# Kernel optimization log

Hardware: AMD Instinct MI355X
Metric: run time of the kernel (lower is better)

## Reference

```python
import jax, jax.numpy as jnp
import numpy as np

NG = 1024      # graphs
NPG = 128      # nodes per graph (forced by lin1 = Linear(128*hid, 128))
N = NG * NPG   # 131072 nodes
DEG = 16       # avg in-graph degree
E = N * DEG    # 2,097,152 edges
IN, H = 4, 64


def setup_inputs() -> dict:
    key = jax.random.key(0)
    ks = jax.random.split(key, 24)
    x = jax.random.normal(ks[0], (N, IN), jnp.float32)
    # edges constrained within each 128-node graph
    src = jax.random.randint(ks[1], (E,), 0, NPG)
    dst = jax.random.randint(ks[2], (E,), 0, NPG)
    off = jnp.repeat(jnp.arange(NG, dtype=jnp.int32) * NPG, NPG * DEG)
    edge_index = jnp.stack([src.astype(jnp.int32) + off, dst.astype(jnp.int32) + off])
    g = lambda k, shp, fan: jax.random.normal(k, shp, jnp.float32) / np.float32(np.sqrt(fan))
    return {
        "x": x, "edge_index": edge_index,
        # GATv2Conv(4->64)
        "Wl": g(ks[3], (IN, H), IN), "bl": jnp.zeros((H,), jnp.float32),
        "Wr": g(ks[4], (IN, H), IN), "br": jnp.zeros((H,), jnp.float32),
        "att_v2": g(ks[5], (H,), H), "b_v2": jnp.zeros((H,), jnp.float32),
        # GATConv #1 (64->64)
        "Wg1": g(ks[6], (H, H), H), "as1": g(ks[7], (H,), H),
        "ad1": g(ks[8], (H,), H), "bg1": jnp.zeros((H,), jnp.float32),
        # GATConv #2 (64->64)
        "Wg2": g(ks[9], (H, H), H), "as2": g(ks[10], (H,), H),
        "ad2": g(ks[11], (H,), H), "bg2": jnp.zeros((H,), jnp.float32),
        # LayerNorm(64)
        "ln_g": jnp.ones((H,), jnp.float32), "ln_b": jnp.zeros((H,), jnp.float32),
        # heads: Linear(128*64 -> 128), Linear(128 -> 1)
        "W1": g(ks[12], (NPG * H, 128), NPG * H), "b1": jnp.zeros((128,), jnp.float32),
        "W2": g(ks[13], (128, 1), 128), "b2": jnp.zeros((1,), jnp.float32),
    }


def _seg_softmax(logits, seg):
    # stable softmax over edges grouped by destination node
    m = jax.ops.segment_max(logits, seg, num_segments=N)
    ex = jnp.exp(logits - m[seg])
    s = jax.ops.segment_sum(ex, seg, num_segments=N)
    return ex / (s[seg] + 1e-16)


def _gatv2(x, src, dst, Wl, bl, Wr, br, att, bias):
    xl = x @ Wl + bl                       # source transform [N,H]
    xr = x @ Wr + br                       # target transform [N,H]
    e = jax.nn.leaky_relu(xl[src] + xr[dst], 0.2) @ att   # [E]
    a = _seg_softmax(e, dst)
    out = jax.ops.segment_sum(a[:, None] * xl[src], dst, num_segments=N)
    return out + bias


def _gat(x, src, dst, W, a_src, a_dst, bias):
    # GATConv default: add self-loops
    loop = jnp.arange(N, dtype=src.dtype)
    s2 = jnp.concatenate([src, loop]); d2 = jnp.concatenate([dst, loop])
    xw = x @ W                             # [N,H]
    al_s = xw @ a_src; al_d = xw @ a_dst   # per-node attention halves [N]
    e = jax.nn.leaky_relu(al_s[s2] + al_d[d2], 0.2)
    a = _seg_softmax(e, d2)
    out = jax.ops.segment_sum(a[:, None] * xw[s2], d2, num_segments=N)
    return out + bias


def _layernorm(x, g, b, eps=1e-5):
    mu = jnp.mean(x, -1, keepdims=True)
    var = jnp.mean(jnp.square(x - mu), -1, keepdims=True)
    return (x - mu) * jax.lax.rsqrt(var + eps) * g + b


def reference(x, edge_index, Wl, bl, Wr, br, att_v2, b_v2,
              Wg1, as1, ad1, bg1, Wg2, as2, ad2, bg2,
              ln_g, ln_b, W1, b1, W2, b2):
    src, dst = edge_index[0], edge_index[1]
    h = jax.nn.leaky_relu(_gatv2(x, src, dst, Wl, bl, Wr, br, att_v2, b_v2), 0.01)
    h = _layernorm(h, ln_g, ln_b)
    h = jax.nn.relu(_gat(h, src, dst, Wg1, as1, ad1, bg1))
    h = jax.nn.relu(_gat(h, src, dst, Wg2, as2, ad2, bg2))
    # linearize: batch is sorted with exactly NPG nodes per graph -> reshape
    h = h.reshape(NG, NPG * H)
    h = jax.nn.leaky_relu(h @ W1 + b1, 0.01)
    return jax.nn.sigmoid(h @ W2 + b2)     # [NG, 1]
```

## Files before the change

kernel.cpp:

```cpp
#include <hip/hip_runtime.h>
#include <hip/hip_bf16.h>

#define NGRAPH 1024
#define NPG 128
#define NTOT (NGRAPH*NPG)
#define EPG 2048
#define ETOT (NTOT*16)
#define HD 64

typedef unsigned int uint;
typedef unsigned short ushort_t;
typedef __attribute__((ext_vector_type(8))) short s8v;
typedef __attribute__((ext_vector_type(4))) float f32x4;

#define MFMA16 __builtin_amdgcn_mfma_f32_16x16x32_bf16

__device__ __forceinline__ float lrelu(float x, float s){ return fmaxf(x, x*s); }
__device__ __forceinline__ float b2lo(uint u){ return __uint_as_float(u << 16); }
__device__ __forceinline__ float b2hi(uint u){ return __uint_as_float(u & 0xFFFF0000u); }
__device__ __forceinline__ uint pkbf(float a, float b){
  union { __hip_bfloat162 h; uint u; } t;
  t.h = __hip_bfloat162{__float2bfloat16(a), __float2bfloat16(b)};
  return t.u;
}
__device__ __forceinline__ ushort_t bfb(float v){
  __hip_bfloat16 h = __float2bfloat16(v);
  union { __hip_bfloat16 h; ushort_t u; } t; t.h = h; return t.u;
}
union U4S8 { uint4 u; s8v s; };
__device__ __forceinline__ s8v bcs8(uint4 u){ U4S8 t; t.u = u; return t.s; }

#define DPP_ADD(v, ctrl) ((v) + __int_as_float(__builtin_amdgcn_update_dpp(0, __float_as_int(v), (ctrl), 0xF, 0xF, false)))

__device__ __forceinline__ int oswz(int r, int p){ return (r<<5) | ((((p>>2) ^ (r & 7))<<2) | (p & 3)); }
__device__ __forceinline__ int obase(int r, int oc){ return (r<<5) | (((oc) ^ (r & 7))<<2); }

#define O_F   0
#define O_W   4096
#define O_EV  6144
#define O_ED  7168
#define O_X   8192
#define O_SOF 8704
#define O_SPO 8833
#define O_NMV 8961
#define O_SSE 9089
#define O_ALS 9217
#define O_ALD 9345
#define O_WAS 9476
#define O_WAD 9540
#define SM_SZ 9604

#define GF32A(s, a) { \
    uint4 q0 = *(uint4*)&SM[O_F + obase((s), 4*hf+0)]; \
    uint4 q1 = *(uint4*)&SM[O_F + obase((s), 4*hf+1)]; \
    c0.x += (a)*b2lo(q0.x); c0.y += (a)*b2hi(q0.x); c0.z += (a)*b2lo(q0.y); c0.w += (a)*b2hi(q0.y); \
    c1.x += (a)*b2lo(q0.z); c1.y += (a)*b2hi(q0.z); c1.z += (a)*b2lo(q0.w); c1.w += (a)*b2hi(q0.w); \
    c2.x += (a)*b2lo(q1.x); c2.y += (a)*b2hi(q1.x); c2.z += (a)*b2lo(q1.y); c2.w += (a)*b2hi(q1.y); \
    c3.x += (a)*b2lo(q1.z); c3.y += (a)*b2hi(q1.z); c3.z += (a)*b2lo(q1.w); c3.w += (a)*b2hi(q1.w); }
#define GF32B(s, a) { \
    uint4 q2 = *(uint4*)&SM[O_F + obase((s), 4*hf+2)]; \
    uint4 q3 = *(uint4*)&SM[O_F + obase((s), 4*hf+3)]; \
    c4.x += (a)*b2lo(q2.x); c4.y += (a)*b2hi(q2.x); c4.z += (a)*b2lo(q2.y); c4.w += (a)*b2hi(q2.y); \
    c5.x += (a)*b2lo(q2.z); c5.y += (a)*b2hi(q2.z); c5.z += (a)*b2lo(q2.w); c5.w += (a)*b2hi(q2.w); \
    c6.x += (a)*b2lo(q3.x); c6.y += (a)*b2hi(q3.x); c6.z += (a)*b2lo(q3.y); c6.w += (a)*b2hi(q3.y); \
    c7.x += (a)*b2lo(q3.z); c7.y += (a)*b2hi(q3.z); c7.z += (a)*b2lo(q3.w); c7.w += (a)*b2hi(q3.w); }
#define GF32(s, a) { GF32A(s, a) __builtin_amdgcn_sched_barrier(0); GF32B(s, a) }

#define STF32(d) { \
    sXl[oswz((d), hf*16+ 0)] = pkbf(c0.x, c0.y); sXl[oswz((d), hf*16+ 1)] = pkbf(c0.z, c0.w); \
    sXl[oswz((d), hf*16+ 2)] = pkbf(c1.x, c1.y); sXl[oswz((d), hf*16+ 3)] = pkbf(c1.z, c1.w); \
    sXl[oswz((d), hf*16+ 4)] = pkbf(c2.x, c2.y); sXl[oswz((d), hf*16+ 5)] = pkbf(c2.z, c2.w); \
    sXl[oswz((d), hf*16+ 6)] = pkbf(c3.x, c3.y); sXl[oswz((d), hf*16+ 7)] = pkbf(c3.z, c3.w); \
    sXl[oswz((d), hf*16+ 8)] = pkbf(c4.x, c4.y); sXl[oswz((d), hf*16+ 9)] = pkbf(c4.z, c4.w); \
    sXl[oswz((d), hf*16+10)] = pkbf(c5.x, c5.y); sXl[oswz((d), hf*16+11)] = pkbf(c5.z, c5.w); \
    sXl[oswz((d), hf*16+12)] = pkbf(c6.x, c6.y); sXl[oswz((d), hf*16+13)] = pkbf(c6.z, c6.w); \
    sXl[oswz((d), hf*16+14)] = pkbf(c7.x, c7.y); sXl[oswz((d), hf*16+15)] = pkbf(c7.z, c7.w); }

__global__ void __launch_bounds__(256) gnn_fused(
    const float* __restrict__ x, const int* __restrict__ ei,
    const float* __restrict__ Wl, const float* __restrict__ bl,
    const float* __restrict__ Wr, const float* __restrict__ br,
    const float* __restrict__ att, const float* __restrict__ bv2,
    const float* __restrict__ Wg1, const float* __restrict__ as1,
    const float* __restrict__ ad1, const float* __restrict__ bg1,
    const float* __restrict__ Wg2, const float* __restrict__ as2,
    const float* __restrict__ ad2, const float* __restrict__ bg2,
    const float* __restrict__ lng, const float* __restrict__ lnb,
    uint* __restrict__ hout)
{
  __shared__ uint SM[SM_SZ];
  uint*      sXl  = SM + O_F;
  _Float16*  evh  = (_Float16*)(SM + O_EV);
  ushort_t*  edsd = (ushort_t*)(SM + O_ED);
  int*       soff = (int*)(SM + O_SOF);
  int*       spos = (int*)(SM + O_SPO);
  float*     nmv  = (float*)(SM + O_NMV);
  float*     sse  = (float*)(SM + O_SSE);
  float*     als  = (float*)(SM + O_ALS);
  float*     ald  = (float*)(SM + O_ALD);
  float*     was  = (float*)(SM + O_WAS);
  float*     wad  = (float*)(SM + O_WAD);
  ushort_t*  sH16 = (ushort_t*)(SM + O_F);
  ushort_t*  wg16 = (ushort_t*)(SM + O_W);
  float*     lgf  = (float*)(SM + O_W);

  const int g    = blockIdx.x;
  const int tid  = threadIdx.x;
  const int lane = tid & 63;
  const int wv   = tid >> 6;
  const int lw   = lane & 15;
  const int lq   = lane >> 4;
  const int oc   = lane & 7;
  const int ebase = g * EPG;

  if (tid < NPG) spos[tid] = 0;
  __syncthreads();
  for (int e = tid; e < EPG; e += 256)
    atomicAdd(&spos[ei[ETOT + ebase + e] - g*NPG], 1);
  __syncthreads();
  if (wv == 0) {
    int c0 = spos[lane], c1 = spos[lane + 64];
    #pragma unroll
    for (int o = 1; o < 64; o <<= 1) { int t = __shfl_up(c0, o); if (lane >= o) c0 += t; }
    #pragma unroll
    for (int o = 1; o < 64; o <<= 1) { int t = __shfl_up(c1, o); if (lane >= o) c1 += t; }
    int tot0 = __shfl(c0, 63);
    soff[lane + 1]  = c0;
    soff[lane + 65] = c1 + tot0;
    if (lane == 0) soff[0] = 0;
  }
  __syncthreads();
  if (tid < NPG) spos[tid] = soff[tid];
  __syncthreads();
  for (int e = tid; e < EPG; e += 256) {
    int s = ei[ebase + e] - g*NPG;
    int d = ei[ETOT + ebase + e] - g*NPG;
    int p = atomicAdd(&spos[d], 1);
    edsd[p] = (ushort_t)(s | (d << 8));
  }

  {
    const float4* x4g = (const float4*)x + (size_t)g * NPG;
    float4* sx4w = (float4*)(SM + O_X);
    if (tid < NPG) sx4w[tid] = x4g[tid];
    const int pl = lane & 31, hb = lane >> 5;
    const float2 wl0 = *(const float2*)&Wl[0*64 + 2*pl];
    const float2 wl1 = *(const float2*)&Wl[1*64 + 2*pl];
    const float2 wl2 = *(const float2*)&Wl[2*64 + 2*pl];
    const float2 wl3 = *(const float2*)&Wl[3*64 + 2*pl];
    const float2 blp = *(const float2*)&bl[2*pl];
    for (int st = 0; st < 16; st++) {
      int i = st*8 + wv*2 + hb;
      float4 xi = x4g[i];
      float l0 = blp.x + xi.x*wl0.x + xi.y*wl1.x + xi.z*wl2.x + xi.w*wl3.x;
      float l1 = blp.y + xi.x*wl0.y + xi.y*wl1.y + xi.z*wl2.y + xi.w*wl3.y;
      sXl[oswz(i, pl)] = pkbf(l0, l1);
    }
  }
  __syncthreads();

  {
    const float4* sx4 = (const float4*)(SM + O_X);
    const int lw16 = lane & 15;
    const int g16  = tid >> 4;
    float4 w0 = *(const float4*)&Wr[0*64 + lw16*4];
    float4 w1 = *(const float4*)&Wr[1*64 + lw16*4];
    float4 w2 = *(const float4*)&Wr[2*64 + lw16*4];
    float4 w3 = *(const float4*)&Wr[3*64 + lw16*4];
    float4 brv = *(const float4*)&br[lw16*4];
    float4 atv = *(const float4*)&att[lw16*4];
    for (int it = 0; it < 8; it++) {
      int d = it*16 + g16;
      float4 xd = sx4[d];
      float4 xr;
      xr.x = brv.x + xd.x*w0.x + xd.y*w1.x + xd.z*w2.x + xd.w*w3.x;
      xr.y = brv.y + xd.x*w0.y + xd.y*w1.y + xd.z*w2.y + xd.w*w3.y;
      xr.z = brv.z + xd.x*w0.z + xd.y*w1.z + xd.z*w2.z + xd.w*w3.z;
      xr.w = brv.w + xd.x*w0.w + xd.y*w1.w + xd.z*w2.w + xd.w*w3.w;
      int p0 = soff[d], p1 = soff[d+1];
      for (int p = p0; p < p1; p++) {
        int s = edsd[p] & 127;
        uint2 ql = *(uint2*)&SM[O_F + oswz(s, 2*lw16)];
        float e, v;
        v = b2lo(ql.x)+xr.x; e  = lrelu(v,0.2f)*atv.x;
        v = b2hi(ql.x)+xr.y; e += lrelu(v,0.2f)*atv.y;
        v = b2lo(ql.y)+xr.z; e += lrelu(v,0.2f)*atv.z;
        v = b2hi(ql.y)+xr.w; e += lrelu(v,0.2f)*atv.w;
        e = DPP_ADD(e, 0x111); e = DPP_ADD(e, 0x112);
        e = DPP_ADD(e, 0x114); e = DPP_ADD(e, 0x118);
        if (lw16 == 15) lgf[p] = e;
      }
    }
  }
  __syncthreads();

  {
    const int g16 = tid >> 4, sl = tid & 15;
    for (int it = 0; it < 8; it++) {
      int d = it*16 + g16;
      int p0 = soff[d], p1 = soff[d+1];
      float m = -1e30f;
      for (int p = p0 + sl; p < p1; p += 16) m = fmaxf(m, lgf[p]);
      #pragma unroll
      for (int o = 1; o < 16; o <<= 1) m = fmaxf(m, __shfl_xor(m, o));
      float ssum = 0.f;
      for (int p = p0 + sl; p < p1; p += 16) {
        float ex = __expf(lgf[p] - m); ssum += ex; evh[p] = (_Float16)ex;
      }
      #pragma unroll
      for (int o = 1; o < 16; o <<= 1) ssum += __shfl_xor(ssum, o);
      if (sl == 0) nmv[d] = 1.f / (ssum + 1e-16f);
    }
  }
  __syncthreads();

  {
    const int d = tid >> 1, hf = tid & 1;
    int p0 = soff[d], p1 = soff[d+1];
    float nmv_d = nmv[d];
    f32x4 c0={0,0,0,0}, c1={0,0,0,0}, c2={0,0,0,0}, c3={0,0,0,0};
    f32x4 c4={0,0,0,0}, c5={0,0,0,0}, c6={0,0,0,0}, c7={0,0,0,0};
    for (int p = p0; p < p1; p++) {
      int s = edsd[p] & 127;
      float a = nmv_d * (float)evh[p];
      GF32(s, a)
    }
    float s1 = 0.f, s2 = 0.f;
    #define BRELN(cv, v) { \
      float4 bq = *(const float4*)&bv2[hf*32 + 4*(v)]; \
      cv.x = lrelu(cv.x + bq.x, 0.01f); cv.y = lrelu(cv.y + bq.y, 0.01f); \
      cv.z = lrelu(cv.z + bq.z, 0.01f); cv.w = lrelu(cv.w + bq.w, 0.01f); \
      s1 += cv.x + cv.y + cv.z + cv.w; \
      s2 += cv.x*cv.x + cv.y*cv.y + cv.z*cv.z + cv.w*cv.w; }
    BRELN(c0,0) BRELN(c1,1) BRELN(c2,2) BRELN(c3,3)
    BRELN(c4,4) BRELN(c5,5) BRELN(c6,6) BRELN(c7,7)
    #undef BRELN
    s1 += __shfl_xor(s1, 1); s2 += __shfl_xor(s2, 1);
    float mu  = s1 * 0.015625f;
    float var = s2 * 0.015625f - mu*mu;
    float rs  = rsqrtf(var + 1e-5f);
    #define LNAP(cv, v) { \
      float4 gq = *(const float4*)&lng[hf*32 + 4*(v)]; \
      float4 bq = *(const float4*)&lnb[hf*32 + 4*(v)]; \
      cv.x = (cv.x-mu)*rs*gq.x + bq.x; cv.y = (cv.y-mu)*rs*gq.y + bq.y; \
      cv.z = (cv.z-mu)*rs*gq.z + bq.z; cv.w = (cv.w-mu)*rs*gq.w + bq.w; }
    LNAP(c0,0) LNAP(c1,1) LNAP(c2,2) LNAP(c3,3)
    LNAP(c4,4) LNAP(c5,5) LNAP(c6,6) LNAP(c7,7)
    #undef LNAP
    __syncthreads();
    STF32(d)
  }
  __syncthreads();

  for (int layer = 0; layer < 2; layer++) {
    const float* Wg  = layer ? Wg2 : Wg1;
    const float* avs = layer ? as2 : as1;
    const float* avd = layer ? ad2 : ad1;
    const float* bg  = layer ? bg2 : bg1;

    if (tid < 128) {
      const float* av = (tid < 64) ? avs : avd;
      float* dst = (tid < 64) ? was : wad;
      int k = tid & 63;
      float acc = 0.f;
      #pragma unroll
      for (int jj = 0; jj < 16; jj++) {
        float4 w = *(const float4*)&Wg[k*64 + jj*4];
        float4 a = *(const float4*)&av[jj*4];
        acc += w.x*a.x + w.y*a.y + w.z*a.z + w.w*a.w;
      }
      dst[k] = acc;
    } else {
      int t2 = tid - 128;
      #pragma unroll
      for (int i = 0; i < 8; i++) {
        int idx = t2 + i*128;
        int k = idx >> 4, j4 = (idx & 15)*4;
        float4 w = *(const float4*)&Wg[k*64 + j4];
        wg16[oswz(j4+0, k>>1)*2 + (k&1)] = bfb(w.x);
        wg16[oswz(j4+1, k>>1)*2 + (k&1)] = bfb(w.y);
        wg16[oswz(j4+2, k>>1)*2 + (k&1)] = bfb(w.z);
        wg16[oswz(j4+3, k>>1)*2 + (k&1)] = bfb(w.w);
      }
    }
    __syncthreads();

    {
      float4 ws0 = *(float4*)&was[oc*8], ws1 = *(float4*)&was[oc*8 + 4];
      float4 wd0 = *(float4*)&wad[oc*8], wd1 = *(float4*)&wad[oc*8 + 4];
      for (int ps = 0; ps < 4; ps++) {
        int n = ps*32 + (tid >> 3);
        uint4 qv = *(uint4*)&SM[O_F + obase(n, oc)];
        float f0=b2lo(qv.x), f1=b2hi(qv.x), f2=b2lo(qv.y), f3=b2hi(qv.y);
        float f4=b2lo(qv.z), f5=b2hi(qv.z), f6=b2lo(qv.w), f7=b2hi(qv.w);
        float sa = f0*ws0.x+f1*ws0.y+f2*ws0.z+f3*ws0.w+f4*ws1.x+f5*ws1.y+f6*ws1.z+f7*ws1.w;
        float sd = f0*wd0.x+f1*wd0.y+f2*wd0.z+f3*wd0.w+f4*wd1.x+f5*wd1.y+f6*wd1.z+f7*wd1.w;
        sa = DPP_ADD(sa, 0x111); sa = DPP_ADD(sa, 0x112); sa = DPP_ADD(sa, 0x114);
        sd = DPP_ADD(sd, 0x111); sd = DPP_ADD(sd, 0x112); sd = DPP_ADD(sd, 0x114);
        if ((lane & 7) == 7) { als[n] = sa; ald[n] = sd; }
      }
    }
    __syncthreads();

    {
      const int r0 = 32*wv;
      uint4 a00 = *(uint4*)&SM[O_F + obase(r0+lw,    lq  )];
      uint4 a01 = *(uint4*)&SM[O_F + obase(r0+lw,    4+lq)];
      uint4 a10 = *(uint4*)&SM[O_F + obase(r0+16+lw, lq  )];
      uint4 a11 = *(uint4*)&SM[O_F + obase(r0+16+lw, 4+lq)];
      #pragma unroll
      for (int nt = 0; nt < 4; nt++) {
        uint4 b0 = *(uint4*)&SM[O_W + obase(nt*16+lw, lq  )];
        uint4 b1 = *(uint4*)&SM[O_W + obase(nt*16+lw, 4+lq)];
        f32x4 z = {0.f,0.f,0.f,0.f};
        f32x4 c0 = MFMA16(bcs8(a00), bcs8(b0), z, 0, 0, 0);
        c0 = MFMA16(bcs8(a01), bcs8(b1), c0, 0, 0, 0);
        f32x4 c1 = MFMA16(bcs8(a10), bcs8(b0), z, 0, 0, 0);
        c1 = MFMA16(bcs8(a11), bcs8(b1), c1, 0, 0, 0);
        int col = nt*16 + lw;
        #pragma unroll
        for (int rg = 0; rg < 4; rg++) {
          sH16[oswz(r0 + lq*4 + rg,      col>>1)*2 + (col&1)] = bfb(c0[rg]);
          sH16[oswz(r0 + 16 + lq*4 + rg, col>>1)*2 + (col&1)] = bfb(c1[rg]);
        }
      }
    }
    {
      const int g16 = tid >> 4, sl = tid & 15;
      for (int it = 0; it < 8; it++) {
        int d = it*16 + g16;
        int p0 = soff[d], p1 = soff[d+1];
        float adv = ald[d];
        float se = lrelu(als[d] + adv, 0.2f);
        float m = se;
        for (int p = p0 + sl; p < p1; p += 16)
          m = fmaxf(m, lrelu(als[edsd[p] & 127] + adv, 0.2f));
        #pragma unroll
        for (int o = 1; o < 16; o <<= 1) m = fmaxf(m, __shfl_xor(m, o));
        float ex0 = __expf(se - m);
        float ssum = 0.f;
        for (int p = p0 + sl; p < p1; p += 16) {
          float ex = __expf(lrelu(als[edsd[p] & 127] + adv, 0.2f) - m);
          ssum += ex; evh[p] = (_Float16)ex;
        }
        #pragma unroll
        for (int o = 1; o < 16; o <<= 1) ssum += __shfl_xor(ssum, o);
        if (sl == 0) { nmv[d] = 1.f / (ssum + ex0 + 1e-16f); sse[d] = ex0; }
      }
    }
    __syncthreads();

    {
      const int d = tid >> 1, hf = tid & 1;
      int p0 = soff[d], p1 = soff[d+1];
      float nmv_d = nmv[d];
      f32x4 c0={0,0,0,0}, c1={0,0,0,0}, c2={0,0,0,0}, c3={0,0,0,0};
      f32x4 c4={0,0,0,0}, c5={0,0,0,0}, c6={0,0,0,0}, c7={0,0,0,0};
      {
        float a0 = sse[d] * nmv_d;
        GF32(d, a0)
      }
      for (int p = p0; p < p1; p++) {
        int s = edsd[p] & 127;
        float a = nmv_d * (float)evh[p];
        GF32(s, a)
      }
      #define BREL2(cv, v) { \
        float4 bq = *(const float4*)&bg[hf*32 + 4*(v)]; \
        cv.x = fmaxf(cv.x + bq.x, 0.f); cv.y = fmaxf(cv.y + bq.y, 0.f); \
        cv.z = fmaxf(cv.z + bq.z, 0.f); cv.w = fmaxf(cv.w + bq.w, 0.f); }
      BREL2(c0,0) BREL2(c1,1) BREL2(c2,2) BREL2(c3,3)
      BREL2(c4,4) BREL2(c5,5) BREL2(c6,6) BREL2(c7,7)
      #undef BREL2
      __syncthreads();
      STF32(d)
    }
    __syncthreads();
  }

  {
    uint* hg = hout + (size_t)g * 4096;
    #pragma unroll
    for (int i = 0; i < 16; i++) {
      int idx = tid + i*256;
      hg[idx] = SM[O_F + oswz(idx >> 5, idx & 31)];
    }
  }
}

__global__ __launch_bounds__(256) void w1_transpose(const float* __restrict__ W1,
                                                    uint* __restrict__ w1t)
{
  __shared__ float sw[64*130];
  const int tid = threadIdx.x;
  const int k0 = blockIdx.x * 64;
  #pragma unroll
  for (int i = 0; i < 8; i++) {
    int idx = tid + i*256;
    int r = idx >> 5, c4 = (idx & 31)*4;
    *(float4*)&sw[r*130 + c4] = *(const float4*)&W1[(size_t)(k0+r)*128 + c4];
  }
  __syncthreads();
  #pragma unroll
  for (int i = 0; i < 16; i++) {
    int idx = tid + i*256;
    int c = idx >> 5, kp = idx & 31;
    w1t[(size_t)c*4096 + (k0>>1) + kp] = pkbf(sw[(2*kp)*130 + c], sw[(2*kp+1)*130 + c]);
  }
}

__global__ __launch_bounds__(256) void head_gemm(
    const uint* __restrict__ hbuf, const uint* __restrict__ w1t,
    float* __restrict__ partial)
{
  __shared__ uint sAh[2048];
  __shared__ uint sBh[4096];
  const int tid = threadIdx.x, lane = tid & 63, wv = tid >> 6;
  const int lw = lane & 15, lq = lane >> 4;
  const int g0 = blockIdx.x * 64;
  const int ks = blockIdx.y;
  f32x4 acc[8];
  #pragma unroll
  for (int i = 0; i < 8; i++) acc[i] = f32x4{0.f,0.f,0.f,0.f};

  for (int ch = 0; ch < 8; ch++) {
    int pb = ks*256 + ch*32;
    #pragma unroll
    for (int i = 0; i < 2; i++) {
      int idx = tid + i*256; int r = idx >> 3, q4 = idx & 7;
      uint4 v = *(const uint4*)&hbuf[(size_t)(g0+r)*4096 + pb + q4*4];
      *(uint4*)&sAh[(r<<5) | ((q4 ^ (r & 7))<<2)] = v;
    }
    #pragma unroll
    for (int i = 0; i < 4; i++) {
      int idx = tid + i*256; int r = idx >> 3, q4 = idx & 7;
      uint4 v = *(const uint4*)&w1t[(size_t)r*4096 + pb + q4*4];
      *(uint4*)&sBh[(r<<5) | ((q4 ^ (r & 7))<<2)] = v;
    }
    __syncthreads();
    int ra = 16*wv + lw;
    s8v a0 = bcs8(*(uint4*)&sAh[obase(ra, lq)]);
    s8v a1 = bcs8(*(uint4*)&sAh[obase(ra, 4+lq)]);
    #pragma unroll
    for (int nt = 0; nt < 8; nt++) {
      int c = nt*16 + lw;
      s8v b0 = bcs8(*(uint4*)&sBh[obase(c, lq)]);
      s8v b1 = bcs8(*(uint4*)&sBh[obase(c, 4+lq)]);
      acc[nt] = MFMA16(a0, b0, acc[nt], 0, 0, 0);
      acc[nt] = MFMA16(a1, b1, acc[nt], 0, 0, 0);
    }
    __syncthreads();
  }
  float* pp = partial + (size_t)ks*131072;
  #pragma unroll
  for (int nt = 0; nt < 8; nt++) {
    int c = nt*16 + lw;
    int r0 = g0 + 16*wv + lq*4;
    #pragma unroll
    for (int rg = 0; rg < 4; rg++)
      pp[(size_t)(r0+rg)*128 + c] = acc[nt][rg];
  }
}

__global__ __launch_bounds__(64) void head_out(
    const float* __restrict__ partial, const float* __restrict__ b1,
    const float* __restrict__ W2, const float* __restrict__ b2,
    float* __restrict__ out)
{
  const int g = blockIdx.x;
  const int l = threadIdx.x;
  float v0 = b1[l], v1 = b1[64 + l];
  #pragma unroll
  for (int s = 0; s < 16; s++) {
    v0 += partial[(size_t)s*131072 + g*128 + l];
    v1 += partial[(size_t)s*131072 + g*128 + 64 + l];
  }
  float sum = lrelu(v0, 0.01f)*W2[l] + lrelu(v1, 0.01f)*W2[64 + l];
  #pragma unroll
  for (int m = 32; m > 0; m >>= 1) sum += __shfl_xor(sum, m);
  if (l == 0) out[g] = 1.f / (1.f + __expf(-(sum + b2[0])));
}

extern "C" void kernel_launch(void* const* d_in, const int* in_sizes, int n_in,
                              void* d_out, int out_size, void* d_ws, size_t ws_size,
                              hipStream_t stream) {
  const float* x   = (const float*)d_in[0];
  const int*   ei  = (const int*)  d_in[1];
  const float* Wl  = (const float*)d_in[2];
  const float* bl_ = (const float*)d_in[3];
  const float* Wr  = (const float*)d_in[4];
  const float* br_ = (const float*)d_in[5];
  const float* att = (const float*)d_in[6];
  const float* bv2 = (const float*)d_in[7];
  const float* Wg1 = (const float*)d_in[8];
  const float* as1 = (const float*)d_in[9];
  const float* ad1 = (const float*)d_in[10];
  const float* bg1 = (const float*)d_in[11];
  const float* Wg2 = (const float*)d_in[12];
  const float* as2 = (const float*)d_in[13];
  const float* ad2 = (const float*)d_in[14];
  const float* bg2 = (const float*)d_in[15];
  const float* lng = (const float*)d_in[16];
  const float* lnb = (const float*)d_in[17];
  const float* W1  = (const float*)d_in[18];
  const float* b1  = (const float*)d_in[19];
  const float* W2  = (const float*)d_in[20];
  const float* b2  = (const float*)d_in[21];
  float* out = (float*)d_out;

  uint*  hbuf    = (uint*)d_ws;
  float* partial = (float*)((char*)d_ws + (size_t)16*1024*1024);
  uint*  w1t     = (uint*)((char*)d_ws + (size_t)24*1024*1024);

  w1_transpose<<<128, 256, 0, stream>>>(W1, w1t);
  gnn_fused<<<NGRAPH, 256, 0, stream>>>(x, ei, Wl, bl_, Wr, br_, att, bv2,
      Wg1, as1, ad1, bg1, Wg2, as2, ad2, bg2, lng, lnb, hbuf);
  head_gemm<<<dim3(16, 16), 256, 0, stream>>>(hbuf, w1t, partial);
  head_out<<<NGRAPH, 64, 0, stream>>>(partial, b1, W2, b2, out);
}
```

Baseline: 309.1 us.

## Split aggregation to four threads per row with staged two-pass output

The attention-weighted aggregation in all three conv layers now uses four threads per destination row, each owning 16 features, instead of two threads owning 32. Each thread handles two rows one after the other. The first row's result goes to a swizzled staging buffer in the weight region, then is copied back after the barrier. This halves the accumulator registers per thread, and `launch_bounds(256,4)` asks for higher occupancy. The cost is serialized per-row gathers, an extra shuffle step for the LayerNorm reduction, and an extra LDS copy pass.

```diff
diff --git a/kernel.cpp b/kernel.cpp
--- a/kernel.cpp
+++ b/kernel.cpp
@@ -34,6 +34,7 @@
 
 __device__ __forceinline__ int oswz(int r, int p){ return (r<<5) | ((((p>>2) ^ (r & 7))<<2) | (p & 3)); }
 __device__ __forceinline__ int obase(int r, int oc){ return (r<<5) | (((oc) ^ (r & 7))<<2); }
+__device__ __forceinline__ int sstg(int r, int c){ return (r<<5) | ((c ^ r) & 31); }
 
 #define O_F   0
 #define O_W   4096
@@ -50,33 +51,26 @@
 #define O_WAD 9540
 #define SM_SZ 9604
 
-#define GF32A(s, a) { \
-    uint4 q0 = *(uint4*)&SM[O_F + obase((s), 4*hf+0)]; \
-    uint4 q1 = *(uint4*)&SM[O_F + obase((s), 4*hf+1)]; \
+#define GF16(s, a) { \
+    uint4 q0 = *(uint4*)&SM[O_F + obase((s), 2*qf+0)]; \
+    uint4 q1 = *(uint4*)&SM[O_F + obase((s), 2*qf+1)]; \
     c0.x += (a)*b2lo(q0.x); c0.y += (a)*b2hi(q0.x); c0.z += (a)*b2lo(q0.y); c0.w += (a)*b2hi(q0.y); \
     c1.x += (a)*b2lo(q0.z); c1.y += (a)*b2hi(q0.z); c1.z += (a)*b2lo(q0.w); c1.w += (a)*b2hi(q0.w); \
     c2.x += (a)*b2lo(q1.x); c2.y += (a)*b2hi(q1.x); c2.z += (a)*b2lo(q1.y); c2.w += (a)*b2hi(q1.y); \
     c3.x += (a)*b2lo(q1.z); c3.y += (a)*b2hi(q1.z); c3.z += (a)*b2lo(q1.w); c3.w += (a)*b2hi(q1.w); }
-#define GF32B(s, a) { \
-    uint4 q2 = *(uint4*)&SM[O_F + obase((s), 4*hf+2)]; \
-    uint4 q3 = *(uint4*)&SM[O_F + obase((s), 4*hf+3)]; \
-    c4.x += (a)*b2lo(q2.x); c4.y += (a)*b2hi(q2.x); c4.z += (a)*b2lo(q2.y); c4.w += (a)*b2hi(q2.y); \
-    c5.x += (a)*b2lo(q2.z); c5.y += (a)*b2hi(q2.z); c5.z += (a)*b2lo(q2.w); c5.w += (a)*b2hi(q2.w); \
-    c6.x += (a)*b2lo(q3.x); c6.y += (a)*b2hi(q3.x); c6.z += (a)*b2lo(q3.y); c6.w += (a)*b2hi(q3.y); \
-    c7.x += (a)*b2lo(q3.z); c7.y += (a)*b2hi(q3.z); c7.z += (a)*b2lo(q3.w); c7.w += (a)*b2hi(q3.w); }
-#define GF32(s, a) { GF32A(s, a) __builtin_amdgcn_sched_barrier(0); GF32B(s, a) }
-
-#define STF32(d) { \
-    sXl[oswz((d), hf*16+ 0)] = pkbf(c0.x, c0.y); sXl[oswz((d), hf*16+ 1)] = pkbf(c0.z, c0.w); \
-    sXl[oswz((d), hf*16+ 2)] = pkbf(c1.x, c1.y); sXl[oswz((d), hf*16+ 3)] = pkbf(c1.z, c1.w); \
-    sXl[oswz((d), hf*16+ 4)] = pkbf(c2.x, c2.y); sXl[oswz((d), hf*16+ 5)] = pkbf(c2.z, c2.w); \
-    sXl[oswz((d), hf*16+ 6)] = pkbf(c3.x, c3.y); sXl[oswz((d), hf*16+ 7)] = pkbf(c3.z, c3.w); \
-    sXl[oswz((d), hf*16+ 8)] = pkbf(c4.x, c4.y); sXl[oswz((d), hf*16+ 9)] = pkbf(c4.z, c4.w); \
-    sXl[oswz((d), hf*16+10)] = pkbf(c5.x, c5.y); sXl[oswz((d), hf*16+11)] = pkbf(c5.z, c5.w); \
-    sXl[oswz((d), hf*16+12)] = pkbf(c6.x, c6.y); sXl[oswz((d), hf*16+13)] = pkbf(c6.z, c6.w); \
-    sXl[oswz((d), hf*16+14)] = pkbf(c7.x, c7.y); sXl[oswz((d), hf*16+15)] = pkbf(c7.z, c7.w); }
-
-__global__ void __launch_bounds__(256) gnn_fused(
+
+#define STF16(d) { \
+    sXl[oswz((d), qf*8+0)] = pkbf(c0.x,c0.y); sXl[oswz((d), qf*8+1)] = pkbf(c0.z,c0.w); \
+    sXl[oswz((d), qf*8+2)] = pkbf(c1.x,c1.y); sXl[oswz((d), qf*8+3)] = pkbf(c1.z,c1.w); \
+    sXl[oswz((d), qf*8+4)] = pkbf(c2.x,c2.y); sXl[oswz((d), qf*8+5)] = pkbf(c2.z,c2.w); \
+    sXl[oswz((d), qf*8+6)] = pkbf(c3.x,c3.y); sXl[oswz((d), qf*8+7)] = pkbf(c3.z,c3.w); }
+#define STG16(d) { \
+    stg[sstg((d), qf*8+0)] = pkbf(c0.x,c0.y); stg[sstg((d), qf*8+1)] = pkbf(c0.z,c0.w); \
+    stg[sstg((d), qf*8+2)] = pkbf(c1.x,c1.y); stg[sstg((d), qf*8+3)] = pkbf(c1.z,c1.w); \
+    stg[sstg((d), qf*8+4)] = pkbf(c2.x,c2.y); stg[sstg((d), qf*8+5)] = pkbf(c2.z,c2.w); \
+    stg[sstg((d), qf*8+6)] = pkbf(c3.x,c3.y); stg[sstg((d), qf*8+7)] = pkbf(c3.z,c3.w); }
+
+__global__ void __launch_bounds__(256, 4) gnn_fused(
     const float* __restrict__ x, const int* __restrict__ ei,
     const float* __restrict__ Wl, const float* __restrict__ bl,
     const float* __restrict__ Wr, const float* __restrict__ br,
@@ -103,6 +97,7 @@
   ushort_t*  sH16 = (ushort_t*)(SM + O_F);
   ushort_t*  wg16 = (ushort_t*)(SM + O_W);
   float*     lgf  = (float*)(SM + O_W);
+  uint*      stg  = SM + O_W;
 
   const int g    = blockIdx.x;
   const int tid  = threadIdx.x;
@@ -161,14 +156,13 @@
 
   {
     const float4* sx4 = (const float4*)(SM + O_X);
-    const int lw16 = lane & 15;
-    const int g16  = tid >> 4;
-    float4 w0 = *(const float4*)&Wr[0*64 + lw16*4];
-    float4 w1 = *(const float4*)&Wr[1*64 + lw16*4];
-    float4 w2 = *(const float4*)&Wr[2*64 + lw16*4];
-    float4 w3 = *(const float4*)&Wr[3*64 + lw16*4];
-    float4 brv = *(const float4*)&br[lw16*4];
-    float4 atv = *(const float4*)&att[lw16*4];
+    const int g16 = tid >> 4;
+    float4 w0 = *(const float4*)&Wr[0*64 + lw*4];
+    float4 w1 = *(const float4*)&Wr[1*64 + lw*4];
+    float4 w2 = *(const float4*)&Wr[2*64 + lw*4];
+    float4 w3 = *(const float4*)&Wr[3*64 + lw*4];
+    float4 brv = *(const float4*)&br[lw*4];
+    float4 atv = *(const float4*)&att[lw*4];
     for (int it = 0; it < 8; it++) {
       int d = it*16 + g16;
       float4 xd = sx4[d];
@@ -180,7 +174,7 @@
       int p0 = soff[d], p1 = soff[d+1];
       for (int p = p0; p < p1; p++) {
         int s = edsd[p] & 127;
-        uint2 ql = *(uint2*)&SM[O_F + oswz(s, 2*lw16)];
+        uint2 ql = *(uint2*)&SM[O_F + oswz(s, 2*lw)];
         float e, v;
         v = b2lo(ql.x)+xr.x; e  = lrelu(v,0.2f)*atv.x;
         v = b2hi(ql.x)+xr.y; e += lrelu(v,0.2f)*atv.y;
@@ -188,7 +182,7 @@
         v = b2hi(ql.y)+xr.w; e += lrelu(v,0.2f)*atv.w;
         e = DPP_ADD(e, 0x111); e = DPP_ADD(e, 0x112);
         e = DPP_ADD(e, 0x114); e = DPP_ADD(e, 0x118);
-        if (lw16 == 15) lgf[p] = e;
+        if (lw == 15) lgf[p] = e;
       }
     }
   }
@@ -215,40 +209,51 @@
   __syncthreads();
 
   {
-    const int d = tid >> 1, hf = tid & 1;
-    int p0 = soff[d], p1 = soff[d+1];
-    float nmv_d = nmv[d];
-    f32x4 c0={0,0,0,0}, c1={0,0,0,0}, c2={0,0,0,0}, c3={0,0,0,0};
-    f32x4 c4={0,0,0,0}, c5={0,0,0,0}, c6={0,0,0,0}, c7={0,0,0,0};
-    for (int p = p0; p < p1; p++) {
-      int s = edsd[p] & 127;
-      float a = nmv_d * (float)evh[p];
-      GF32(s, a)
-    }
-    float s1 = 0.f, s2 = 0.f;
-    #define BRELN(cv, v) { \
-      float4 bq = *(const float4*)&bv2[hf*32 + 4*(v)]; \
-      cv.x = lrelu(cv.x + bq.x, 0.01f); cv.y = lrelu(cv.y + bq.y, 0.01f); \
-      cv.z = lrelu(cv.z + bq.z, 0.01f); cv.w = lrelu(cv.w + bq.w, 0.01f); \
-      s1 += cv.x + cv.y + cv.z + cv.w; \
-      s2 += cv.x*cv.x + cv.y*cv.y + cv.z*cv.z + cv.w*cv.w; }
-    BRELN(c0,0) BRELN(c1,1) BRELN(c2,2) BRELN(c3,3)
-    BRELN(c4,4) BRELN(c5,5) BRELN(c6,6) BRELN(c7,7)
-    #undef BRELN
-    s1 += __shfl_xor(s1, 1); s2 += __shfl_xor(s2, 1);
-    float mu  = s1 * 0.015625f;
-    float var = s2 * 0.015625f - mu*mu;
-    float rs  = rsqrtf(var + 1e-5f);
-    #define LNAP(cv, v) { \
-      float4 gq = *(const float4*)&lng[hf*32 + 4*(v)]; \
-      float4 bq = *(const float4*)&lnb[hf*32 + 4*(v)]; \
-      cv.x = (cv.x-mu)*rs*gq.x + bq.x; cv.y = (cv.y-mu)*rs*gq.y + bq.y; \
-      cv.z = (cv.z-mu)*rs*gq.z + bq.z; cv.w = (cv.w-mu)*rs*gq.w + bq.w; }
-    LNAP(c0,0) LNAP(c1,1) LNAP(c2,2) LNAP(c3,3)
-    LNAP(c4,4) LNAP(c5,5) LNAP(c6,6) LNAP(c7,7)
-    #undef LNAP
-    __syncthreads();
-    STF32(d)
+    const int rr = tid >> 2, qf = tid & 3;
+    auto doRow = [&](int d, int toStage) {
+      int p0 = soff[d], p1 = soff[d+1];
+      float nmv_d = nmv[d];
+      f32x4 c0={0,0,0,0}, c1={0,0,0,0}, c2={0,0,0,0}, c3={0,0,0,0};
+      for (int p = p0; p < p1; p++) {
+        int s = edsd[p] & 127;
+        float a = nmv_d * (float)evh[p];
+        GF16(s, a)
+      }
+      float s1 = 0.f, s2 = 0.f;
+      #define BRELN(cv, j) { \
+        float4 bq = *(const float4*)&bv2[qf*16 + 4*(j)]; \
+        cv.x = lrelu(cv.x + bq.x, 0.01f); cv.y = lrelu(cv.y + bq.y, 0.01f); \
+        cv.z = lrelu(cv.z + bq.z, 0.01f); cv.w = lrelu(cv.w + bq.w, 0.01f); \
+        s1 += cv.x + cv.y + cv.z + cv.w; \
+        s2 += cv.x*cv.x + cv.y*cv.y + cv.z*cv.z + cv.w*cv.w; }
+      BRELN(c0,0) BRELN(c1,1) BRELN(c2,2) BRELN(c3,3)
+      #undef BRELN
+      s1 += __shfl_xor(s1, 1); s2 += __shfl_xor(s2, 1);
+      s1 += __shfl_xor(s1, 2); s2 += __shfl_xor(s2, 2);
+      float mu  = s1 * 0.015625f;
+      float var = s2 * 0.015625f - mu*mu;
+      float rs  = rsqrtf(var + 1e-5f);
+      #define LNAP(cv, j) { \
+        float4 gq = *(const float4*)&lng[qf*16 + 4*(j)]; \
+        float4 bq = *(const float4*)&lnb[qf*16 + 4*(j)]; \
+        cv.x = (cv.x-mu)*rs*gq.x + bq.x; cv.y = (cv.y-mu)*rs*gq.y + bq.y; \
+        cv.z = (cv.z-mu)*rs*gq.z + bq.z; cv.w = (cv.w-mu)*rs*gq.w + bq.w; }
+      LNAP(c0,0) LNAP(c1,1) LNAP(c2,2) LNAP(c3,3)
+      #undef LNAP
+      if (toStage) {
+        STG16(d)
+      } else {
+        __syncthreads();
+        STF16(d)
+      }
+    };
+    doRow(rr, 1);
+    doRow(64 + rr, 0);
+    #pragma unroll
+    for (int i = 0; i < 8; i++) {
+      int idx = tid + i*256; int r = idx >> 5, c = idx & 31;
+      sXl[oswz(r, c)] = stg[sstg(r, c)];
+    }
   }
   __syncthreads();
 
@@ -351,29 +356,40 @@
     __syncthreads();
 
     {
-      const int d = tid >> 1, hf = tid & 1;
-      int p0 = soff[d], p1 = soff[d+1];
-      float nmv_d = nmv[d];
-      f32x4 c0={0,0,0,0}, c1={0,0,0,0}, c2={0,0,0,0}, c3={0,0,0,0};
-      f32x4 c4={0,0,0,0}, c5={0,0,0,0}, c6={0,0,0,0}, c7={0,0,0,0};
-      {
-        float a0 = sse[d] * nmv_d;
-        GF32(d, a0)
-      }
-      for (int p = p0; p < p1; p++) {
-        int s = edsd[p] & 127;
-        float a = nmv_d * (float)evh[p];
-        GF32(s, a)
-      }
-      #define BREL2(cv, v) { \
-        float4 bq = *(const float4*)&bg[hf*32 + 4*(v)]; \
-        cv.x = fmaxf(cv.x + bq.x, 0.f); cv.y = fmaxf(cv.y + bq.y, 0.f); \
-        cv.z = fmaxf(cv.z + bq.z, 0.f); cv.w = fmaxf(cv.w + bq.w, 0.f); }
-      BREL2(c0,0) BREL2(c1,1) BREL2(c2,2) BREL2(c3,3)
-      BREL2(c4,4) BREL2(c5,5) BREL2(c6,6) BREL2(c7,7)
-      #undef BREL2
-      __syncthreads();
-      STF32(d)
+      const int rr = tid >> 2, qf = tid & 3;
+      auto doRow = [&](int d, int toStage) {
+        int p0 = soff[d], p1 = soff[d+1];
+        float nmv_d = nmv[d];
+        f32x4 c0={0,0,0,0}, c1={0,0,0,0}, c2={0,0,0,0}, c3={0,0,0,0};
+        {
+          float a0 = sse[d] * nmv_d;
+          GF16(d, a0)
+        }
+        for (int p = p0; p < p1; p++) {
+          int s = edsd[p] & 127;
+          float a = nmv_d * (float)evh[p];
+          GF16(s, a)
+        }
+        #define BREL2(cv, j) { \
+          float4 bq = *(const float4*)&bg[qf*16 + 4*(j)]; \
+          cv.x = fmaxf(cv.x + bq.x, 0.f); cv.y = fmaxf(cv.y + bq.y, 0.f); \
+          cv.z = fmaxf(cv.z + bq.z, 0.f); cv.w = fmaxf(cv.w + bq.w, 0.f); }
+        BREL2(c0,0) BREL2(c1,1) BREL2(c2,2) BREL2(c3,3)
+        #undef BREL2
+        if (toStage) {
+          STG16(d)
+        } else {
+          __syncthreads();
+          STF16(d)
+        }
+      };
+      doRow(rr, 1);
+      doRow(64 + rr, 0);
+      #pragma unroll
+      for (int i = 0; i < 8; i++) {
+        int idx = tid + i*256; int r = idx >> 5, c = idx & 31;
+        sXl[oswz(r, c)] = stg[sstg(r, c)];
+      }
     }
     __syncthreads();
   }
```

Result: faster. 285.9 us (-7.5%).
